# Kernel tuning notes

Measured on AMD Instinct MI355X. Metric: run time of the kernel, lower is better.

Reference implementation:

```python
import jax, jax.numpy as jnp
import numpy as np

ROBOT_W = 1.0
PHASE_W = 1.0
COHER_W = 10.0
SPEED_W = 5.0
MAX_SPEED = 10.0
SMOOTH_VEL_W = 0.05
SMOOTH_ACC_W = 0.01

# illegal phase transitions {(0,2),(1,0),(2,0),(2,1)} as a 3x3 lookup table
_ILLEGAL = np.zeros((3, 3), dtype=bool)
for a, b in [(0, 2), (1, 0), (2, 0), (2, 1)]:
    _ILLEGAL[a, b] = True
ILLEGAL_TABLE = jnp.asarray(_ILLEGAL)


def setup_inputs() -> dict:
    key = jax.random.key(0)
    k1, k2, k3, k4 = jax.random.split(key, 4)
    B, T = 256, 8192
    # scale by 8 so per-frame speeds (norm of diffs of 3-vectors) exceed MAX_SPEED
    pred_robot = jax.random.normal(k1, (B, T, 12), dtype=jnp.float32) * 8.0
    gt_robot = jax.random.normal(k2, (B, T, 12), dtype=jnp.float32) * 8.0
    pred_phase = jax.random.normal(k3, (B, T, 3), dtype=jnp.float32)
    gt_phase = jax.random.randint(k4, (B, T), 0, 3, dtype=jnp.int32)
    return {"pred_robot": pred_robot, "pred_phase": pred_phase,
            "gt_robot": gt_robot, "gt_phase": gt_phase}


def _coherence_loss(phase_logits):
    # vectorized replacement for the O(B*T) Python double loop
    p = jnp.argmax(phase_logits, axis=-1)            # [B, T]
    pt, pt1 = p[:, :-1], p[:, 1:]                    # [B, T-1]
    illegal = ILLEGAL_TABLE[pt, pt1]                 # [B, T-1] bool
    # logit of the (illegal) predicted phase at t+1
    sel = jnp.take_along_axis(phase_logits[:, 1:], pt1[..., None], axis=-1)[..., 0]
    loss_sum = jnp.sum(jnp.where(illegal, sel * sel, 0.0))
    count = jnp.sum(illegal)
    return jnp.where(count > 0, loss_sum / jnp.maximum(count, 1).astype(sel.dtype), 0.0)


def _speed_loss(pred_robot):
    B, T, D = pred_robot.shape
    vel = pred_robot[:, 1:] - pred_robot[:, :-1]     # [B, T-1, 12]
    pts = vel.reshape(B, T - 1, 4, 3)
    speeds = jnp.linalg.norm(pts, axis=-1)           # [B, T-1, 4]
    pen = jax.nn.relu(speeds - MAX_SPEED)
    return SPEED_W * jnp.mean(pen * pen)


def reference(pred_robot, pred_phase, gt_robot, gt_phase):
    # MSE over robot trajectory
    robot_loss = jnp.mean((pred_robot - gt_robot) ** 2)
    # cross-entropy over 3 phase classes
    logp = jax.nn.log_softmax(pred_phase, axis=-1)   # [B, T, 3]
    nll = -jnp.take_along_axis(logp, gt_phase[..., None].astype(jnp.int32), axis=-1)[..., 0]
    phase_loss = jnp.mean(nll)
    coherence = _coherence_loss(pred_phase)
    speed_loss = _speed_loss(pred_robot)
    vel = pred_robot[:, 1:] - pred_robot[:, :-1]
    vel_loss = jnp.mean(vel * vel)
    acc = pred_robot[:, 2:] - 2.0 * pred_robot[:, 1:-1] + pred_robot[:, :-2]
    acc_loss = jnp.mean(acc * acc)
    total = (ROBOT_W * robot_loss + PHASE_W * phase_loss + COHER_W * coherence
             + speed_loss + SMOOTH_VEL_W * vel_loss + SMOOTH_ACC_W * acc_loss)
    return total
```

## Files before the change

### kernel.cpp

```cpp
#include <hip/hip_runtime.h>
#include <math.h>

#define B_DIM 256
#define T_DIM 8192
#define BLOCK 256
#define NSLOT 256
#define GRID_BLOCKS 8192


__global__ __launch_bounds__(BLOCK) void combined_loss_main(
    const float4* __restrict__ pred4,
    const float*  __restrict__ pred_phase,
    const float4* __restrict__ gt4,
    const int*    __restrict__ gt_phase,
    double* __restrict__ ws)
{
    __shared__ float s_red[4][8];

    const int tid = threadIdx.x;
    const int r   = (int)blockIdx.x * BLOCK + tid;
    const int t   = r & (T_DIM - 1);
    const bool v1 = (t < T_DIM - 1);
    const bool v2 = (t < T_DIM - 2);

    const float4* pr = pred4 + (size_t)r * 3;
    const float4* gr = gt4   + (size_t)r * 3;
    const float*  pp = pred_phase + (size_t)r * 3;

    const int o1 = v1 ? 3 : 0;
    const int o2 = v2 ? 6 : 0;

    float4 a0 = pr[0],      a1 = pr[1],      a2 = pr[2];
    float4 b0 = pr[o1],     b1 = pr[o1 + 1], b2 = pr[o1 + 2];
    float4 c0 = pr[o2],     c1 = pr[o2 + 1], c2 = pr[o2 + 2];
    float4 q0 = gr[0],      q1 = gr[1],      q2 = gr[2];

    const float l0 = pp[0],  l1 = pp[1],  l2 = pp[2];
    const float n0 = pp[o1], n1 = pp[o1 + 1], n2 = pp[o1 + 2];
    const int gidx = gt_phase[r];

    float sse = 0.0f;
    {
        float d;
        d = a0.x - q0.x; sse += d*d;  d = a0.y - q0.y; sse += d*d;
        d = a0.z - q0.z; sse += d*d;  d = a0.w - q0.w; sse += d*d;
        d = a1.x - q1.x; sse += d*d;  d = a1.y - q1.y; sse += d*d;
        d = a1.z - q1.z; sse += d*d;  d = a1.w - q1.w; sse += d*d;
        d = a2.x - q2.x; sse += d*d;  d = a2.y - q2.y; sse += d*d;
        d = a2.z - q2.z; sse += d*d;  d = a2.w - q2.w; sse += d*d;
    }

    float m = fmaxf(l0, fmaxf(l1, l2));
    float lse = m + logf(expf(l0 - m) + expf(l1 - m) + expf(l2 - m));
    float sel = (gidx == 0) ? l0 : ((gidx == 1) ? l1 : l2);
    float nll = lse - sel;

    float csum = 0.0f, ccnt = 0.0f;
    if (v1) {
        int p = 0; float pm = l0;
        if (l1 > pm) { pm = l1; p = 1; }
        if (l2 > pm) { pm = l2; p = 2; }
        int p1 = 0; float m1 = n0;
        if (n1 > m1) { m1 = n1; p1 = 1; }
        if (n2 > m1) { m1 = n2; p1 = 2; }
        int mask = (p == 0) ? 4 : ((p == 1) ? 1 : 3);
        if ((mask >> p1) & 1) { csum = m1 * m1; ccnt = 1.0f; }
    }

    float pen2 = 0.0f, velsq = 0.0f, accsq = 0.0f;
    {
        float rA[12] = { a0.x,a0.y,a0.z,a0.w, a1.x,a1.y,a1.z,a1.w, a2.x,a2.y,a2.z,a2.w };
        float rB[12] = { b0.x,b0.y,b0.z,b0.w, b1.x,b1.y,b1.z,b1.w, b2.x,b2.y,b2.z,b2.w };
        float rC[12] = { c0.x,c0.y,c0.z,c0.w, c1.x,c1.y,c1.z,c1.w, c2.x,c2.y,c2.z,c2.w };

        if (v1) {
            float vel[12];
            #pragma unroll
            for (int k = 0; k < 12; ++k) { vel[k] = rB[k] - rA[k]; velsq += vel[k]*vel[k]; }

            #pragma unroll
            for (int j = 0; j < 4; ++j) {
                float sx = vel[3*j], sy = vel[3*j+1], sz = vel[3*j+2];
                float sp = sqrtf(sx*sx + sy*sy + sz*sz);
                float d = sp - 10.0f;
                if (d > 0.0f) pen2 += d*d;
            }

            if (v2) {
                #pragma unroll
                for (int k = 0; k < 12; ++k) {
                    float a = rC[k] - 2.0f*rB[k] + rA[k];
                    accsq += a*a;
                }
            }
        }
    }

    float vals[7] = { sse, nll, csum, ccnt, pen2, velsq, accsq };
    #pragma unroll
    for (int off = 32; off > 0; off >>= 1) {
        #pragma unroll
        for (int q = 0; q < 7; ++q)
            vals[q] += __shfl_down(vals[q], off, 64);
    }
    const int wave = tid >> 6, lane = tid & 63;
    if (lane == 0) {
        #pragma unroll
        for (int q = 0; q < 7; ++q) s_red[wave][q] = vals[q];
    }
    __syncthreads();
    if (tid < 7) {
        double acc = (double)s_red[0][tid] + (double)s_red[1][tid]
                   + (double)s_red[2][tid] + (double)s_red[3][tid];
        atomicAdd(&ws[(size_t)(blockIdx.x & (NSLOT - 1)) * 8 + tid], acc);
    }
}

__global__ __launch_bounds__(256) void combined_loss_final(
    const double* __restrict__ ws, float* __restrict__ out)
{
    __shared__ double sred[4][7];
    const int tid = threadIdx.x;
    double v[7];
    #pragma unroll
    for (int q = 0; q < 7; ++q) v[q] = ws[(size_t)tid * 8 + q];
    #pragma unroll
    for (int off = 32; off > 0; off >>= 1) {
        #pragma unroll
        for (int q = 0; q < 7; ++q)
            v[q] += __shfl_down(v[q], off, 64);
    }
    const int wave = tid >> 6, lane = tid & 63;
    if (lane == 0) {
        #pragma unroll
        for (int q = 0; q < 7; ++q) sred[wave][q] = v[q];
    }
    __syncthreads();
    if (tid == 0) {
        double s[7];
        #pragma unroll
        for (int q = 0; q < 7; ++q)
            s[q] = sred[0][q] + sred[1][q] + sred[2][q] + sred[3][q];
        const double robot = s[0] / (double)((size_t)B_DIM * T_DIM * 12);
        const double phase = s[1] / (double)((size_t)B_DIM * T_DIM);
        const double coher = (s[3] > 0.0) ? (s[2] / fmax(s[3], 1.0)) : 0.0;
        const double speed = 5.0  * (s[4] / (double)((size_t)B_DIM * (T_DIM - 1) * 4));
        const double vel   = 0.05 * (s[5] / (double)((size_t)B_DIM * (T_DIM - 1) * 12));
        const double acc   = 0.01 * (s[6] / (double)((size_t)B_DIM * (T_DIM - 2) * 12));
        out[0] = (float)(robot + phase + 10.0 * coher + speed + vel + acc);
    }
}

extern "C" void kernel_launch(void* const* d_in, const int* in_sizes, int n_in,
                              void* d_out, int out_size, void* d_ws, size_t ws_size,
                              hipStream_t stream)
{
    const float4* pred4      = (const float4*)d_in[0];
    const float*  pred_phase = (const float*)d_in[1];
    const float4* gt4        = (const float4*)d_in[2];
    const int*    gt_phase   = (const int*)d_in[3];
    double* ws  = (double*)d_ws;
    float*  out = (float*)d_out;

    hipMemsetAsync(d_ws, 0, (size_t)NSLOT * 8 * sizeof(double), stream);

    combined_loss_main<<<dim3(GRID_BLOCKS), BLOCK, 0, stream>>>(pred4, pred_phase, gt4, gt_phase, ws);
    combined_loss_final<<<1, 256, 0, stream>>>(ws, out);
}
```

Baseline: 240.4 us.

## Remap threads to float4 granularity for coalesced loads with shared-memory neighbor carry

Each thread now handles individual float4 chunks (four per thread) instead of a whole 12-float row, so global loads of pred/gt are fully coalesced across lanes. Per-point speed norms that straddle float4 boundaries are stitched together through a shared-memory carry array, and the phase logits are read as float4 with neighbor values exchanged through shared memory. The robot and phase sums are folded into one accumulator to shorten the reduction. This adds shared-memory traffic, extra syncs and complex index math (div by 3) in exchange for better memory access patterns on a bandwidth-bound kernel.

```diff
diff --git a/kernel.cpp b/kernel.cpp
--- a/kernel.cpp
+++ b/kernel.cpp
@@ -5,149 +5,253 @@
 #define T_DIM 8192
 #define BLOCK 256
 #define NSLOT 256
-#define GRID_BLOCKS 8192
-
+#define K_PRED 4
+#define NPB (BLOCK * K_PRED)
+#define NF4 (B_DIM * T_DIM * 3)
+#define NPH4 (NF4 / 4)
+#define GRID_BLOCKS (NF4 / NPB)
+
+
+__device__ __forceinline__ unsigned div3u(unsigned x) {
+    return __umulhi(x, 0xAAAAAAABu) >> 1;
+}
+__device__ __forceinline__ float pen_term(float s) {
+    float d = fmaxf(sqrtf(s) - 10.0f, 0.0f);
+    return d * d;
+}
+__device__ __forceinline__ void argmax3(float l0, float l1, float l2, int &p, float &m) {
+    p = 0; m = l0;
+    if (l1 > m) { m = l1; p = 1; }
+    if (l2 > m) { m = l2; p = 2; }
+}
+__device__ __forceinline__ float nll3(float l0, float l1, float l2, int g) {
+    float mx = fmaxf(l0, fmaxf(l1, l2));
+    float lse = mx + logf(expf(l0 - mx) + expf(l1 - mx) + expf(l2 - mx));
+    float sel = (g == 0) ? l0 : ((g == 1) ? l1 : l2);
+    return lse - sel;
+}
 
 __global__ __launch_bounds__(BLOCK) void combined_loss_main(
     const float4* __restrict__ pred4,
-    const float*  __restrict__ pred_phase,
+    const float4* __restrict__ ph4,
     const float4* __restrict__ gt4,
     const int*    __restrict__ gt_phase,
     double* __restrict__ ws)
 {
-    __shared__ float s_red[4][8];
+    __shared__ float  s_carry[NPB + 1];
+    __shared__ float2 s_zw[BLOCK + 1];
+    __shared__ float  s_pm_m[BLOCK + 1];
+    __shared__ int    s_pm_p[BLOCK + 1];
+    __shared__ float  s_red[4][6];
 
     const int tid = threadIdx.x;
-    const int r   = (int)blockIdx.x * BLOCK + tid;
-    const int t   = r & (T_DIM - 1);
-    const bool v1 = (t < T_DIM - 1);
-    const bool v2 = (t < T_DIM - 2);
-
-    const float4* pr = pred4 + (size_t)r * 3;
-    const float4* gr = gt4   + (size_t)r * 3;
-    const float*  pp = pred_phase + (size_t)r * 3;
-
-    const int o1 = v1 ? 3 : 0;
-    const int o2 = v2 ? 6 : 0;
-
-    float4 a0 = pr[0],      a1 = pr[1],      a2 = pr[2];
-    float4 b0 = pr[o1],     b1 = pr[o1 + 1], b2 = pr[o1 + 2];
-    float4 c0 = pr[o2],     c1 = pr[o2 + 1], c2 = pr[o2 + 2];
-    float4 q0 = gr[0],      q1 = gr[1],      q2 = gr[2];
-
-    const float l0 = pp[0],  l1 = pp[1],  l2 = pp[2];
-    const float n0 = pp[o1], n1 = pp[o1 + 1], n2 = pp[o1 + 2];
-    const int gidx = gt_phase[r];
-
-    float sse = 0.0f;
+    const int blk = blockIdx.x;
+    const unsigned base = (unsigned)blk * NPB;
+
+    float sse = 0.f, velsq = 0.f, accsq = 0.f;
+    float loc[K_PRED], car[K_PRED];
+    unsigned c0v = 0;
+
+    #pragma unroll
+    for (int k = 0; k < K_PRED; ++k) {
+        const unsigned i = base + (unsigned)(k * BLOCK) + tid;
+        const unsigned r = div3u(i);
+        const unsigned c = i - 3u * r;
+        if (k == 0) c0v = c;
+        const unsigned t = r & (T_DIM - 1);
+        const bool v1 = t < (T_DIM - 1);
+        const bool v2 = t < (T_DIM - 2);
+        const unsigned i3 = v1 ? i + 3u : i;
+        const unsigned i6 = v2 ? i + 6u : i;
+
+        const float4 A  = pred4[i];
+        const float4 G  = gt4[i];
+        const float4 A3 = pred4[i3];
+        const float4 A6 = pred4[i6];
+
+        float d;
+        d = A.x - G.x; sse = fmaf(d, d, sse);
+        d = A.y - G.y; sse = fmaf(d, d, sse);
+        d = A.z - G.z; sse = fmaf(d, d, sse);
+        d = A.w - G.w; sse = fmaf(d, d, sse);
+
+        float sqx = 0.f, sqy = 0.f, sqz = 0.f, sqw = 0.f;
+        if (v1) {
+            const float vx = A3.x - A.x, vy = A3.y - A.y, vz = A3.z - A.z, vw = A3.w - A.w;
+            sqx = vx * vx; sqy = vy * vy; sqz = vz * vz; sqw = vw * vw;
+            velsq += sqx + sqy + sqz + sqw;
+        }
+        if (v2) {
+            float a;
+            a = A6.x - 2.0f * A3.x + A.x; accsq = fmaf(a, a, accsq);
+            a = A6.y - 2.0f * A3.y + A.y; accsq = fmaf(a, a, accsq);
+            a = A6.z - 2.0f * A3.z + A.z; accsq = fmaf(a, a, accsq);
+            a = A6.w - 2.0f * A3.w + A.w; accsq = fmaf(a, a, accsq);
+        }
+        float l3v, crv;
+        if (c == 0)      { l3v = sqx + sqy + sqz; crv = sqw; }
+        else if (c == 1) { l3v = sqz + sqw;       crv = sqx + sqy; }
+        else             { l3v = sqy + sqz + sqw; crv = sqx; }
+        loc[k] = l3v; car[k] = crv;
+        s_carry[k * BLOCK + tid] = crv;
+    }
+
+    const unsigned j = (unsigned)blk * BLOCK + tid;
+    const float4 P = ph4[j];
+    s_zw[tid + 1] = make_float2(P.z, P.w);
+
+    if (tid == 0) {
+        float2 zwp = make_float2(0.f, 0.f);
+        if (j != 0) {
+            const float2* ph2 = (const float2*)ph4;
+            zwp = ph2[2u * j - 1u];
+        }
+        s_zw[0] = zwp;
+        float crs = 0.f;
+        const unsigned ib = base + NPB;
+        if (ib < (unsigned)NF4) {
+            const unsigned rb = div3u(ib);
+            const unsigned cb = ib - 3u * rb;
+            const unsigned tb = rb & (T_DIM - 1);
+            if (tb < (T_DIM - 1)) {
+                const float4 Ab  = pred4[ib];
+                const float4 Ab3 = pred4[ib + 3u];
+                const float bx = Ab3.x - Ab.x, by = Ab3.y - Ab.y;
+                const float bz = Ab3.z - Ab.z, bw = Ab3.w - Ab.w;
+                const float sx = bx * bx, sy = by * by, sx2 = bz * bz, sw = bw * bw;
+                (void)sx2;
+                crs = (cb == 0) ? sw : ((cb == 1) ? (sx + sy) : sx);
+            }
+        }
+        s_carry[NPB] = crs;
+    }
+    __syncthreads();
+
+    const unsigned g   = div3u(j);
+    const unsigned dph = j - 3u * g;
+    const float2 zwp = s_zw[tid];
+    float l0, l1, l2;
+    if (dph == 0)      { l0 = P.x;   l1 = P.y;   l2 = P.z; }
+    else if (dph == 1) { l0 = zwp.y; l1 = P.x;   l2 = P.y; }
+    else               { l0 = zwp.x; l1 = zwp.y; l2 = P.x; }
+    const unsigned prow = 4u * g + dph;
+
+    int gA, gB = 0;
+    if (dph == 2) {
+        const int2 gg = ((const int2*)gt_phase)[prow >> 1];
+        gA = gg.x; gB = gg.y;
+    } else {
+        gA = gt_phase[prow];
+    }
+    float nll = nll3(l0, l1, l2, gA);
+    int pP; float mP;
+    argmax3(l0, l1, l2, pP, mP);
+    s_pm_m[tid] = mP; s_pm_p[tid] = pP;
+
+    int p3 = 0; float m3 = 0.f;
+    if (dph == 2) {
+        nll += nll3(P.y, P.z, P.w, gB);
+        argmax3(P.y, P.z, P.w, p3, m3);
+    }
+    if (tid == BLOCK - 1) {
+        float mS = 0.f; int pS = 0;
+        const unsigned jn = j + 1u;
+        if (jn < (unsigned)NPH4) {
+            const float4 Pn = ph4[jn];
+            const unsigned gn = div3u(jn);
+            const unsigned dn = jn - 3u * gn;
+            float a0, a1, a2;
+            if (dn == 0)      { a0 = Pn.x; a1 = Pn.y; a2 = Pn.z; }
+            else if (dn == 1) { a0 = P.w;  a1 = Pn.x; a2 = Pn.y; }
+            else              { a0 = P.z;  a1 = P.w;  a2 = Pn.x; }
+            argmax3(a0, a1, a2, pS, mS);
+        }
+        s_pm_m[BLOCK] = mS; s_pm_p[BLOCK] = pS;
+    }
+    __syncthreads();
+
+    float csum = 0.f, ccnt = 0.f;
     {
-        float d;
-        d = a0.x - q0.x; sse += d*d;  d = a0.y - q0.y; sse += d*d;
-        d = a0.z - q0.z; sse += d*d;  d = a0.w - q0.w; sse += d*d;
-        d = a1.x - q1.x; sse += d*d;  d = a1.y - q1.y; sse += d*d;
-        d = a1.z - q1.z; sse += d*d;  d = a1.w - q1.w; sse += d*d;
-        d = a2.x - q2.x; sse += d*d;  d = a2.y - q2.y; sse += d*d;
-        d = a2.z - q2.z; sse += d*d;  d = a2.w - q2.w; sse += d*d;
-    }
-
-    float m = fmaxf(l0, fmaxf(l1, l2));
-    float lse = m + logf(expf(l0 - m) + expf(l1 - m) + expf(l2 - m));
-    float sel = (gidx == 0) ? l0 : ((gidx == 1) ? l1 : l2);
-    float nll = lse - sel;
-
-    float csum = 0.0f, ccnt = 0.0f;
-    if (v1) {
-        int p = 0; float pm = l0;
-        if (l1 > pm) { pm = l1; p = 1; }
-        if (l2 > pm) { pm = l2; p = 2; }
-        int p1 = 0; float m1 = n0;
-        if (n1 > m1) { m1 = n1; p1 = 1; }
-        if (n2 > m1) { m1 = n2; p1 = 2; }
-        int mask = (p == 0) ? 4 : ((p == 1) ? 1 : 3);
-        if ((mask >> p1) & 1) { csum = m1 * m1; ccnt = 1.0f; }
-    }
-
-    float pen2 = 0.0f, velsq = 0.0f, accsq = 0.0f;
-    {
-        float rA[12] = { a0.x,a0.y,a0.z,a0.w, a1.x,a1.y,a1.z,a1.w, a2.x,a2.y,a2.z,a2.w };
-        float rB[12] = { b0.x,b0.y,b0.z,b0.w, b1.x,b1.y,b1.z,b1.w, b2.x,b2.y,b2.z,b2.w };
-        float rC[12] = { c0.x,c0.y,c0.z,c0.w, c1.x,c1.y,c1.z,c1.w, c2.x,c2.y,c2.z,c2.w };
-
-        if (v1) {
-            float vel[12];
-            #pragma unroll
-            for (int k = 0; k < 12; ++k) { vel[k] = rB[k] - rA[k]; velsq += vel[k]*vel[k]; }
-
-            #pragma unroll
-            for (int j = 0; j < 4; ++j) {
-                float sx = vel[3*j], sy = vel[3*j+1], sz = vel[3*j+2];
-                float sp = sqrtf(sx*sx + sy*sy + sz*sz);
-                float d = sp - 10.0f;
-                if (d > 0.0f) pen2 += d*d;
+        const float mN = s_pm_m[tid + 1];
+        const int   pN = s_pm_p[tid + 1];
+        const unsigned t1 = prow & (T_DIM - 1);
+        if (t1 < (T_DIM - 1)) {
+            const int   pB2 = (dph == 2) ? p3 : pN;
+            const float mB2 = (dph == 2) ? m3 : mN;
+            const int mask = (pP == 0) ? 4 : ((pP == 1) ? 1 : 3);
+            if ((mask >> pB2) & 1) { csum += mB2 * mB2; ccnt += 1.f; }
+        }
+        if (dph == 2) {
+            const unsigned t2 = (prow + 1u) & (T_DIM - 1);
+            if (t2 < (T_DIM - 1)) {
+                const int mask = (p3 == 0) ? 4 : ((p3 == 1) ? 1 : 3);
+                if ((mask >> pN) & 1) { csum += mN * mN; ccnt += 1.f; }
             }
-
-            if (v2) {
-                #pragma unroll
-                for (int k = 0; k < 12; ++k) {
-                    float a = rC[k] - 2.0f*rB[k] + rA[k];
-                    accsq += a*a;
-                }
-            }
-        }
-    }
-
-    float vals[7] = { sse, nll, csum, ccnt, pen2, velsq, accsq };
+        }
+    }
+
+    float pen2 = 0.f;
+    #pragma unroll
+    for (int k = 0; k < K_PRED; ++k) {
+        unsigned ck = c0v + (unsigned)k;
+        if (ck >= 3u) ck -= 3u;
+        const float up = s_carry[k * BLOCK + tid + 1];
+        const float a = loc[k] + ((ck == 1u) ? up : 0.f);
+        const float b = (ck == 0u) ? (car[k] + up) : 0.f;
+        pen2 += pen_term(a) + pen_term(b);
+    }
+
+    float vals[6] = { fmaf(12.0f, nll, sse), csum, ccnt, pen2, velsq, accsq };
     #pragma unroll
     for (int off = 32; off > 0; off >>= 1) {
         #pragma unroll
-        for (int q = 0; q < 7; ++q)
+        for (int q = 0; q < 6; ++q)
             vals[q] += __shfl_down(vals[q], off, 64);
     }
     const int wave = tid >> 6, lane = tid & 63;
     if (lane == 0) {
         #pragma unroll
-        for (int q = 0; q < 7; ++q) s_red[wave][q] = vals[q];
-    }
-    __syncthreads();
-    if (tid < 7) {
-        double acc = (double)s_red[0][tid] + (double)s_red[1][tid]
-                   + (double)s_red[2][tid] + (double)s_red[3][tid];
-        atomicAdd(&ws[(size_t)(blockIdx.x & (NSLOT - 1)) * 8 + tid], acc);
+        for (int q = 0; q < 6; ++q) s_red[wave][q] = vals[q];
+    }
+    __syncthreads();
+    if (tid < 6) {
+        const double acc = (double)s_red[0][tid] + (double)s_red[1][tid]
+                         + (double)s_red[2][tid] + (double)s_red[3][tid];
+        atomicAdd(&ws[(size_t)(blk & (NSLOT - 1)) * 8 + tid], acc);
     }
 }
 
 __global__ __launch_bounds__(256) void combined_loss_final(
     const double* __restrict__ ws, float* __restrict__ out)
 {
-    __shared__ double sred[4][7];
+    __shared__ double sred[4][6];
     const int tid = threadIdx.x;
-    double v[7];
-    #pragma unroll
-    for (int q = 0; q < 7; ++q) v[q] = ws[(size_t)tid * 8 + q];
+    double v[6];
+    #pragma unroll
+    for (int q = 0; q < 6; ++q) v[q] = ws[(size_t)tid * 8 + q];
     #pragma unroll
     for (int off = 32; off > 0; off >>= 1) {
         #pragma unroll
-        for (int q = 0; q < 7; ++q)
+        for (int q = 0; q < 6; ++q)
             v[q] += __shfl_down(v[q], off, 64);
     }
     const int wave = tid >> 6, lane = tid & 63;
     if (lane == 0) {
         #pragma unroll
-        for (int q = 0; q < 7; ++q) sred[wave][q] = v[q];
+        for (int q = 0; q < 6; ++q) sred[wave][q] = v[q];
     }
     __syncthreads();
     if (tid == 0) {
-        double s[7];
-        #pragma unroll
-        for (int q = 0; q < 7; ++q)
+        double s[6];
+        #pragma unroll
+        for (int q = 0; q < 6; ++q)
             s[q] = sred[0][q] + sred[1][q] + sred[2][q] + sred[3][q];
-        const double robot = s[0] / (double)((size_t)B_DIM * T_DIM * 12);
-        const double phase = s[1] / (double)((size_t)B_DIM * T_DIM);
-        const double coher = (s[3] > 0.0) ? (s[2] / fmax(s[3], 1.0)) : 0.0;
-        const double speed = 5.0  * (s[4] / (double)((size_t)B_DIM * (T_DIM - 1) * 4));
-        const double vel   = 0.05 * (s[5] / (double)((size_t)B_DIM * (T_DIM - 1) * 12));
-        const double acc   = 0.01 * (s[6] / (double)((size_t)B_DIM * (T_DIM - 2) * 12));
-        out[0] = (float)(robot + phase + 10.0 * coher + speed + vel + acc);
+        const double robot_phase = s[0] / (double)((size_t)B_DIM * T_DIM * 12);
+        const double coher = (s[2] > 0.0) ? (s[1] / fmax(s[2], 1.0)) : 0.0;
+        const double speed = 5.0  * (s[3] / (double)((size_t)B_DIM * (T_DIM - 1) * 4));
+        const double vel   = 0.05 * (s[4] / (double)((size_t)B_DIM * (T_DIM - 1) * 12));
+        const double acc   = 0.01 * (s[5] / (double)((size_t)B_DIM * (T_DIM - 2) * 12));
+        out[0] = (float)(robot_phase + 10.0 * coher + speed + vel + acc);
     }
 }
 
@@ -156,7 +260,7 @@
                               hipStream_t stream)
 {
     const float4* pred4      = (const float4*)d_in[0];
-    const float*  pred_phase = (const float*)d_in[1];
+    const float4* ph4        = (const float4*)d_in[1];
     const float4* gt4        = (const float4*)d_in[2];
     const int*    gt_phase   = (const int*)d_in[3];
     double* ws  = (double*)d_ws;
@@ -164,6 +268,6 @@
 
     hipMemsetAsync(d_ws, 0, (size_t)NSLOT * 8 * sizeof(double), stream);
 
-    combined_loss_main<<<dim3(GRID_BLOCKS), BLOCK, 0, stream>>>(pred4, pred_phase, gt4, gt_phase, ws);
+    combined_loss_main<<<dim3(GRID_BLOCKS), BLOCK, 0, stream>>>(pred4, ph4, gt4, gt_phase, ws);
     combined_loss_final<<<1, 256, 0, stream>>>(ws, out);
 }
```

Measured after the change: 241.9 us. About the same (+0.6%).

## Stage rows through shared memory with coalesced loads and persistent prefetching blocks

Applied to the files above, without the earlier changes.

Replaces per-thread strided loads of three neighbouring rows with coalesced float4 tile loads into LDS, plus a small halo, so neighbour rows for velocity and acceleration are read from shared memory instead of re-fetched from global memory. Switches to a persistent grid of 1024 blocks, each looping over 8 tiles with register double-buffering of the next tile's loads. Also folds phase NLL into the MSE accumulator, cutting one reduction channel, and uses fast exp/log intrinsics. Adds two barriers per tile and register pressure from the prefetch stage, and the fast intrinsics slightly change numerics.

```diff
diff --git a/kernel.cpp b/kernel.cpp
--- a/kernel.cpp
+++ b/kernel.cpp
@@ -5,149 +5,221 @@
 #define T_DIM 8192
 #define BLOCK 256
 #define NSLOT 256
-#define GRID_BLOCKS 8192
-
+#define NBLK  1024
+#define ROWS_TOT (B_DIM * T_DIM)
+#define NTILES (ROWS_TOT / BLOCK)
+#define NT_PER (NTILES / NBLK)
+#define NF4  (ROWS_TOT * 3)
+#define NPH4 (ROWS_TOT * 3 / 4)
+
+
+struct Stage {
+    float4 A0, A1, A2;
+    float4 G0, G1, G2;
+    float4 At;
+    float4 Ph;
+    int    gph;
+};
+
+__device__ __forceinline__ Stage load_tile(int tile, int tid,
+    const float4* __restrict__ pred4, const float4* __restrict__ gt4,
+    const float4* __restrict__ ph4,   const int* __restrict__ gtp)
+{
+    Stage st;
+    const int R = tile * BLOCK;
+    const size_t b4 = (size_t)R * 3;
+
+    st.A0 = pred4[b4 + tid];        st.G0 = gt4[b4 + tid];
+    st.A1 = pred4[b4 + tid + 256];  st.G1 = gt4[b4 + tid + 256];
+    st.A2 = pred4[b4 + tid + 512];  st.G2 = gt4[b4 + tid + 512];
+
+    if (tid < 6) {
+        size_t it4 = b4 + 768 + tid;
+        if (it4 > (size_t)(NF4 - 1)) it4 = (size_t)(NF4 - 1);
+        st.At = pred4[it4];
+    } else {
+        st.At = make_float4(0.f, 0.f, 0.f, 0.f);
+    }
+
+    const size_t p4 = (size_t)192 * tile;
+    const int phcnt = (p4 + 193 <= (size_t)NPH4) ? 193 : 192;
+    st.Ph = (tid < phcnt) ? ph4[p4 + tid] : make_float4(0.f, 0.f, 0.f, 0.f);
+
+    st.gph = gtp[R + tid];
+    return st;
+}
+
+__device__ __forceinline__ float pen_term(float s) {
+    float d = fmaxf(sqrtf(s) - 10.0f, 0.0f);
+    return d * d;
+}
+__device__ __forceinline__ void argmax3(float l0, float l1, float l2, int &p, float &m) {
+    p = 0; m = l0;
+    if (l1 > m) { m = l1; p = 1; }
+    if (l2 > m) { m = l2; p = 2; }
+}
+__device__ __forceinline__ float nll3(float l0, float l1, float l2, int g) {
+    float mx = fmaxf(l0, fmaxf(l1, l2));
+    float s = __expf(l0 - mx) + __expf(l1 - mx) + __expf(l2 - mx);
+    float sel = (g == 0) ? l0 : ((g == 1) ? l1 : l2);
+    return mx + __logf(s) - sel;
+}
 
 __global__ __launch_bounds__(BLOCK) void combined_loss_main(
     const float4* __restrict__ pred4,
-    const float*  __restrict__ pred_phase,
+    const float4* __restrict__ ph4,
     const float4* __restrict__ gt4,
     const int*    __restrict__ gt_phase,
     double* __restrict__ ws)
 {
-    __shared__ float s_red[4][8];
+    __shared__ float4 s_pred[774];
+    __shared__ float4 s_ph4[194];
+    __shared__ float  s_red[4][6];
+    const float* s_ph = (const float*)s_ph4;
 
     const int tid = threadIdx.x;
-    const int r   = (int)blockIdx.x * BLOCK + tid;
-    const int t   = r & (T_DIM - 1);
-    const bool v1 = (t < T_DIM - 1);
-    const bool v2 = (t < T_DIM - 2);
-
-    const float4* pr = pred4 + (size_t)r * 3;
-    const float4* gr = gt4   + (size_t)r * 3;
-    const float*  pp = pred_phase + (size_t)r * 3;
-
-    const int o1 = v1 ? 3 : 0;
-    const int o2 = v2 ? 6 : 0;
-
-    float4 a0 = pr[0],      a1 = pr[1],      a2 = pr[2];
-    float4 b0 = pr[o1],     b1 = pr[o1 + 1], b2 = pr[o1 + 2];
-    float4 c0 = pr[o2],     c1 = pr[o2 + 1], c2 = pr[o2 + 2];
-    float4 q0 = gr[0],      q1 = gr[1],      q2 = gr[2];
-
-    const float l0 = pp[0],  l1 = pp[1],  l2 = pp[2];
-    const float n0 = pp[o1], n1 = pp[o1 + 1], n2 = pp[o1 + 2];
-    const int gidx = gt_phase[r];
-
-    float sse = 0.0f;
-    {
-        float d;
-        d = a0.x - q0.x; sse += d*d;  d = a0.y - q0.y; sse += d*d;
-        d = a0.z - q0.z; sse += d*d;  d = a0.w - q0.w; sse += d*d;
-        d = a1.x - q1.x; sse += d*d;  d = a1.y - q1.y; sse += d*d;
-        d = a1.z - q1.z; sse += d*d;  d = a1.w - q1.w; sse += d*d;
-        d = a2.x - q2.x; sse += d*d;  d = a2.y - q2.y; sse += d*d;
-        d = a2.z - q2.z; sse += d*d;  d = a2.w - q2.w; sse += d*d;
-    }
-
-    float m = fmaxf(l0, fmaxf(l1, l2));
-    float lse = m + logf(expf(l0 - m) + expf(l1 - m) + expf(l2 - m));
-    float sel = (gidx == 0) ? l0 : ((gidx == 1) ? l1 : l2);
-    float nll = lse - sel;
-
-    float csum = 0.0f, ccnt = 0.0f;
-    if (v1) {
-        int p = 0; float pm = l0;
-        if (l1 > pm) { pm = l1; p = 1; }
-        if (l2 > pm) { pm = l2; p = 2; }
-        int p1 = 0; float m1 = n0;
-        if (n1 > m1) { m1 = n1; p1 = 1; }
-        if (n2 > m1) { m1 = n2; p1 = 2; }
-        int mask = (p == 0) ? 4 : ((p == 1) ? 1 : 3);
-        if ((mask >> p1) & 1) { csum = m1 * m1; ccnt = 1.0f; }
-    }
-
-    float pen2 = 0.0f, velsq = 0.0f, accsq = 0.0f;
-    {
-        float rA[12] = { a0.x,a0.y,a0.z,a0.w, a1.x,a1.y,a1.z,a1.w, a2.x,a2.y,a2.z,a2.w };
-        float rB[12] = { b0.x,b0.y,b0.z,b0.w, b1.x,b1.y,b1.z,b1.w, b2.x,b2.y,b2.z,b2.w };
-        float rC[12] = { c0.x,c0.y,c0.z,c0.w, c1.x,c1.y,c1.z,c1.w, c2.x,c2.y,c2.z,c2.w };
-
-        if (v1) {
-            float vel[12];
-            #pragma unroll
-            for (int k = 0; k < 12; ++k) { vel[k] = rB[k] - rA[k]; velsq += vel[k]*vel[k]; }
-
-            #pragma unroll
-            for (int j = 0; j < 4; ++j) {
-                float sx = vel[3*j], sy = vel[3*j+1], sz = vel[3*j+2];
-                float sp = sqrtf(sx*sx + sy*sy + sz*sz);
-                float d = sp - 10.0f;
-                if (d > 0.0f) pen2 += d*d;
+    const int blk = blockIdx.x;
+
+    float sse = 0.f, nll = 0.f, csum = 0.f, ccnt = 0.f;
+    float pen2 = 0.f, velsq = 0.f, accsq = 0.f;
+
+    Stage cur = load_tile(blk, tid, pred4, gt4, ph4, gt_phase);
+
+    for (int it = 0; it < NT_PER; ++it) {
+        const int tile = it * NBLK + blk;
+
+        __syncthreads();
+        s_pred[tid]       = cur.A0;
+        s_pred[tid + 256] = cur.A1;
+        s_pred[tid + 512] = cur.A2;
+        if (tid < 6)   s_pred[768 + tid] = cur.At;
+        if (tid < 193) s_ph4[tid] = cur.Ph;
+        {
+            float d;
+            d = cur.A0.x - cur.G0.x; sse = fmaf(d, d, sse);
+            d = cur.A0.y - cur.G0.y; sse = fmaf(d, d, sse);
+            d = cur.A0.z - cur.G0.z; sse = fmaf(d, d, sse);
+            d = cur.A0.w - cur.G0.w; sse = fmaf(d, d, sse);
+            d = cur.A1.x - cur.G1.x; sse = fmaf(d, d, sse);
+            d = cur.A1.y - cur.G1.y; sse = fmaf(d, d, sse);
+            d = cur.A1.z - cur.G1.z; sse = fmaf(d, d, sse);
+            d = cur.A1.w - cur.G1.w; sse = fmaf(d, d, sse);
+            d = cur.A2.x - cur.G2.x; sse = fmaf(d, d, sse);
+            d = cur.A2.y - cur.G2.y; sse = fmaf(d, d, sse);
+            d = cur.A2.z - cur.G2.z; sse = fmaf(d, d, sse);
+            d = cur.A2.w - cur.G2.w; sse = fmaf(d, d, sse);
+        }
+        const int gph = cur.gph;
+        __syncthreads();
+
+        Stage nxt;
+        if (it + 1 < NT_PER) nxt = load_tile((it + 1) * NBLK + blk, tid, pred4, gt4, ph4, gt_phase);
+        else                 nxt = cur;
+
+        const int t  = (tile * BLOCK + tid) & (T_DIM - 1);
+        const bool v1 = t < (T_DIM - 1);
+        const bool v2 = t < (T_DIM - 2);
+        const int l3 = 3 * tid;
+
+        const float4 r0a = s_pred[l3],     r0b = s_pred[l3 + 1], r0c = s_pred[l3 + 2];
+        const float4 r1a = s_pred[l3 + 3], r1b = s_pred[l3 + 4], r1c = s_pred[l3 + 5];
+        const float4 r2a = s_pred[l3 + 6], r2b = s_pred[l3 + 7], r2c = s_pred[l3 + 8];
+
+        {
+            const float v0 = r1a.x - r0a.x, v1f = r1a.y - r0a.y, v2f = r1a.z - r0a.z, v3 = r1a.w - r0a.w;
+            const float v4 = r1b.x - r0b.x, v5  = r1b.y - r0b.y, v6  = r1b.z - r0b.z, v7 = r1b.w - r0b.w;
+            const float v8 = r1c.x - r0c.x, v9  = r1c.y - r0c.y, v10 = r1c.z - r0c.z, v11 = r1c.w - r0c.w;
+            const float q0 = v0*v0, q1 = v1f*v1f, q2 = v2f*v2f, q3 = v3*v3;
+            const float q4 = v4*v4, q5 = v5*v5,   q6 = v6*v6,   q7 = v7*v7;
+            const float q8 = v8*v8, q9 = v9*v9,   q10 = v10*v10, q11 = v11*v11;
+            if (v1) {
+                velsq += (q0+q1+q2+q3) + (q4+q5+q6+q7) + (q8+q9+q10+q11);
+                pen2  += pen_term(q0+q1+q2) + pen_term(q3+q4+q5)
+                       + pen_term(q6+q7+q8) + pen_term(q9+q10+q11);
             }
-
-            if (v2) {
-                #pragma unroll
-                for (int k = 0; k < 12; ++k) {
-                    float a = rC[k] - 2.0f*rB[k] + rA[k];
-                    accsq += a*a;
-                }
+        }
+        if (v2) {
+            float a;
+            a = r2a.x - 2.0f*r1a.x + r0a.x; accsq = fmaf(a, a, accsq);
+            a = r2a.y - 2.0f*r1a.y + r0a.y; accsq = fmaf(a, a, accsq);
+            a = r2a.z - 2.0f*r1a.z + r0a.z; accsq = fmaf(a, a, accsq);
+            a = r2a.w - 2.0f*r1a.w + r0a.w; accsq = fmaf(a, a, accsq);
+            a = r2b.x - 2.0f*r1b.x + r0b.x; accsq = fmaf(a, a, accsq);
+            a = r2b.y - 2.0f*r1b.y + r0b.y; accsq = fmaf(a, a, accsq);
+            a = r2b.z - 2.0f*r1b.z + r0b.z; accsq = fmaf(a, a, accsq);
+            a = r2b.w - 2.0f*r1b.w + r0b.w; accsq = fmaf(a, a, accsq);
+            a = r2c.x - 2.0f*r1c.x + r0c.x; accsq = fmaf(a, a, accsq);
+            a = r2c.y - 2.0f*r1c.y + r0c.y; accsq = fmaf(a, a, accsq);
+            a = r2c.z - 2.0f*r1c.z + r0c.z; accsq = fmaf(a, a, accsq);
+            a = r2c.w - 2.0f*r1c.w + r0c.w; accsq = fmaf(a, a, accsq);
+        }
+        {
+            const float p00 = s_ph[l3], p01 = s_ph[l3 + 1], p02 = s_ph[l3 + 2];
+            nll += nll3(p00, p01, p02, gph);
+            if (v1) {
+                const float p10 = s_ph[l3 + 3], p11 = s_ph[l3 + 4], p12 = s_ph[l3 + 5];
+                int pP, pN; float mP, mN;
+                argmax3(p00, p01, p02, pP, mP);
+                argmax3(p10, p11, p12, pN, mN);
+                const int mask = (pP == 0) ? 4 : ((pP == 1) ? 1 : 3);
+                if ((mask >> pN) & 1) { csum += mN * mN; ccnt += 1.f; }
             }
         }
-    }
-
-    float vals[7] = { sse, nll, csum, ccnt, pen2, velsq, accsq };
+
+        cur = nxt;
+    }
+
+    float vals[6] = { fmaf(12.0f, nll, sse), csum, ccnt, pen2, velsq, accsq };
     #pragma unroll
     for (int off = 32; off > 0; off >>= 1) {
         #pragma unroll
-        for (int q = 0; q < 7; ++q)
+        for (int q = 0; q < 6; ++q)
             vals[q] += __shfl_down(vals[q], off, 64);
     }
     const int wave = tid >> 6, lane = tid & 63;
     if (lane == 0) {
         #pragma unroll
-        for (int q = 0; q < 7; ++q) s_red[wave][q] = vals[q];
+        for (int q = 0; q < 6; ++q) s_red[wave][q] = vals[q];
     }
     __syncthreads();
-    if (tid < 7) {
-        double acc = (double)s_red[0][tid] + (double)s_red[1][tid]
-                   + (double)s_red[2][tid] + (double)s_red[3][tid];
-        atomicAdd(&ws[(size_t)(blockIdx.x & (NSLOT - 1)) * 8 + tid], acc);
+    if (tid < 6) {
+        const double acc = (double)s_red[0][tid] + (double)s_red[1][tid]
+                         + (double)s_red[2][tid] + (double)s_red[3][tid];
+        atomicAdd(&ws[(size_t)(blk & (NSLOT - 1)) * 8 + tid], acc);
     }
 }
 
 __global__ __launch_bounds__(256) void combined_loss_final(
     const double* __restrict__ ws, float* __restrict__ out)
 {
-    __shared__ double sred[4][7];
+    __shared__ double sred[4][6];
     const int tid = threadIdx.x;
-    double v[7];
+    double v[6];
     #pragma unroll
-    for (int q = 0; q < 7; ++q) v[q] = ws[(size_t)tid * 8 + q];
+    for (int q = 0; q < 6; ++q) v[q] = ws[(size_t)tid * 8 + q];
     #pragma unroll
     for (int off = 32; off > 0; off >>= 1) {
         #pragma unroll
-        for (int q = 0; q < 7; ++q)
+        for (int q = 0; q < 6; ++q)
             v[q] += __shfl_down(v[q], off, 64);
     }
     const int wave = tid >> 6, lane = tid & 63;
     if (lane == 0) {
         #pragma unroll
-        for (int q = 0; q < 7; ++q) sred[wave][q] = v[q];
+        for (int q = 0; q < 6; ++q) sred[wave][q] = v[q];
     }
     __syncthreads();
     if (tid == 0) {
-        double s[7];
-        #pragma unroll
-        for (int q = 0; q < 7; ++q)
+        double s[6];
+        #pragma unroll
+        for (int q = 0; q < 6; ++q)
             s[q] = sred[0][q] + sred[1][q] + sred[2][q] + sred[3][q];
-        const double robot = s[0] / (double)((size_t)B_DIM * T_DIM * 12);
-        const double phase = s[1] / (double)((size_t)B_DIM * T_DIM);
-        const double coher = (s[3] > 0.0) ? (s[2] / fmax(s[3], 1.0)) : 0.0;
-        const double speed = 5.0  * (s[4] / (double)((size_t)B_DIM * (T_DIM - 1) * 4));
-        const double vel   = 0.05 * (s[5] / (double)((size_t)B_DIM * (T_DIM - 1) * 12));
-        const double acc   = 0.01 * (s[6] / (double)((size_t)B_DIM * (T_DIM - 2) * 12));
-        out[0] = (float)(robot + phase + 10.0 * coher + speed + vel + acc);
+        const double robot_phase = s[0] / (double)((size_t)B_DIM * T_DIM * 12);
+        const double coher = (s[2] > 0.0) ? (s[1] / fmax(s[2], 1.0)) : 0.0;
+        const double speed = 5.0  * (s[3] / (double)((size_t)B_DIM * (T_DIM - 1) * 4));
+        const double vel   = 0.05 * (s[4] / (double)((size_t)B_DIM * (T_DIM - 1) * 12));
+        const double acc   = 0.01 * (s[5] / (double)((size_t)B_DIM * (T_DIM - 2) * 12));
+        out[0] = (float)(robot_phase + 10.0 * coher + speed + vel + acc);
     }
 }
 
@@ -156,7 +228,7 @@
                               hipStream_t stream)
 {
     const float4* pred4      = (const float4*)d_in[0];
-    const float*  pred_phase = (const float*)d_in[1];
+    const float4* ph4        = (const float4*)d_in[1];
     const float4* gt4        = (const float4*)d_in[2];
     const int*    gt_phase   = (const int*)d_in[3];
     double* ws  = (double*)d_ws;
@@ -164,6 +236,6 @@
 
     hipMemsetAsync(d_ws, 0, (size_t)NSLOT * 8 * sizeof(double), stream);
 
-    combined_loss_main<<<dim3(GRID_BLOCKS), BLOCK, 0, stream>>>(pred4, pred_phase, gt4, gt_phase, ws);
+    combined_loss_main<<<dim3(NBLK), BLOCK, 0, stream>>>(pred4, ph4, gt4, gt_phase, ws);
     combined_loss_final<<<1, 256, 0, stream>>>(ws, out);
 }
```

New measurement: 244.2 us. About the same (+1.5%).
